# Performance work log

Measured on AMD Instinct MI355X. Metric: run time of the kernel, lower is better.

Reference implementation:

```python
import jax, jax.numpy as jnp
import numpy as np

D_MODEL = 1024
NUM_HEADS = 16
HEAD_DIM = D_MODEL // NUM_HEADS
D_FF = 4 * D_MODEL


def _linear_params(key, d_in, d_out):
    kw, kb = jax.random.split(key)
    bound = 1.0 / np.sqrt(d_in)
    W = jax.random.uniform(kw, (d_in, d_out), minval=-bound, maxval=bound, dtype=jnp.float32)
    b = jax.random.uniform(kb, (d_out,), minval=-bound, maxval=bound, dtype=jnp.float32)
    return W, b


def setup_inputs() -> dict:
    key = jax.random.key(0)
    ks = jax.random.split(key, 6)
    x = jax.random.normal(ks[0], (4, 2048, D_MODEL), dtype=jnp.float32)
    qkv_w, qkv_b = _linear_params(ks[1], D_MODEL, 3 * D_MODEL)
    out_w, out_b = _linear_params(ks[2], D_MODEL, D_MODEL)
    ffn1_w, ffn1_b = _linear_params(ks[3], D_MODEL, D_FF)
    ffn2_w, ffn2_b = _linear_params(ks[4], D_FF, D_MODEL)
    ln1_g = jnp.ones((D_MODEL,), jnp.float32); ln1_b = jnp.zeros((D_MODEL,), jnp.float32)
    ln2_g = jnp.ones((D_MODEL,), jnp.float32); ln2_b = jnp.zeros((D_MODEL,), jnp.float32)
    return {
        "x": x,
        "qkv_w": qkv_w, "qkv_b": qkv_b,
        "out_w": out_w, "out_b": out_b,
        "ffn1_w": ffn1_w, "ffn1_b": ffn1_b,
        "ffn2_w": ffn2_w, "ffn2_b": ffn2_b,
        "ln1_g": ln1_g, "ln1_b": ln1_b,
        "ln2_g": ln2_g, "ln2_b": ln2_b,
    }


def _layer_norm(x, g, b, eps=1e-5):
    mu = jnp.mean(x, axis=-1, keepdims=True)
    var = jnp.mean(jnp.square(x - mu), axis=-1, keepdims=True)
    return (x - mu) * jax.lax.rsqrt(var + eps) * g + b


def reference(x, qkv_w, qkv_b, out_w, out_b, ffn1_w, ffn1_b, ffn2_w, ffn2_b,
              ln1_g, ln1_b, ln2_g, ln2_b):
    B, S, D = x.shape
    H, Hd = NUM_HEADS, HEAD_DIM
    normed = _layer_norm(x, ln1_g, ln1_b)
    qkv = normed @ qkv_w + qkv_b                      # [B,S,3D]
    qkv = qkv.reshape(B, S, 3, H, Hd)
    q = jnp.transpose(qkv[:, :, 0], (0, 2, 1, 3))     # [B,H,S,Hd]
    k = jnp.transpose(qkv[:, :, 1], (0, 2, 1, 3))
    v = jnp.transpose(qkv[:, :, 2], (0, 2, 1, 3))
    scores = jnp.einsum('bhqd,bhkd->bhqk', q, k) / np.sqrt(Hd).astype(np.float32)
    causal = jnp.tril(jnp.ones((S, S), dtype=bool))
    scores = jnp.where(causal[None, None], scores, -jnp.inf)
    attn = jax.nn.softmax(scores, axis=-1)
    attn_out = jnp.einsum('bhqk,bhkd->bhqd', attn, v)  # [B,H,S,Hd]
    attn_out = jnp.transpose(attn_out, (0, 2, 1, 3)).reshape(B, S, D)
    attn_out = attn_out @ out_w + out_b
    x = x + attn_out
    h = _layer_norm(x, ln2_g, ln2_b)
    h = jax.nn.gelu(h @ ffn1_w + ffn1_b, approximate=False)
    h = h @ ffn2_w + ffn2_b
    return x + h
```

## Files before the change

### kernel.cpp

```cpp
#include <hip/hip_runtime.h>
#include <hip/hip_bf16.h>
#include <math.h>

typedef __attribute__((ext_vector_type(8))) short short8;
typedef __attribute__((ext_vector_type(4))) float f32x4;

__device__ __forceinline__ float bf2f(unsigned short u) {
    union { unsigned int i; float f; } c; c.i = ((unsigned int)u) << 16; return c.f;
}
__device__ __forceinline__ unsigned short f2bf(float f) {
    union { float f; unsigned int i; } c; c.f = f;
    unsigned int i = c.i;
    unsigned int r = (i + 0x7FFFu + ((i >> 16) & 1u)) >> 16;
    return (unsigned short)r;
}
__device__ __forceinline__ float fexp2(float x) { return __builtin_amdgcn_exp2f(x); }

__device__ __forceinline__ void gload16(const unsigned short* g, unsigned short* l) {
    __builtin_amdgcn_global_load_lds(
        (const __attribute__((address_space(1))) unsigned int*)g,
        (__attribute__((address_space(3))) unsigned int*)l, 16, 0, 0);
}

__device__ __forceinline__ void load8(const unsigned short* p, float* v) {
    short8 s = *(const short8*)p;
#pragma unroll
    for (int i = 0; i < 8; i++) v[i] = bf2f((unsigned short)s[i]);
}
__device__ __forceinline__ void load8(const float* p, float* v) {
    f32x4 a = ((const f32x4*)p)[0], b = ((const f32x4*)p)[1];
    v[0] = a[0]; v[1] = a[1]; v[2] = a[2]; v[3] = a[3];
    v[4] = b[0]; v[5] = b[1]; v[6] = b[2]; v[7] = b[3];
}
__device__ __forceinline__ void store8(unsigned short* p, const float* v) {
    short8 s;
#pragma unroll
    for (int i = 0; i < 8; i++) s[i] = (short)f2bf(v[i]);
    *(short8*)p = s;
}
__device__ __forceinline__ void store8(float* p, const float* v) {
    f32x4 a, b;
    a[0] = v[0]; a[1] = v[1]; a[2] = v[2]; a[3] = v[3];
    b[0] = v[4]; b[1] = v[5]; b[2] = v[6]; b[3] = v[7];
    ((f32x4*)p)[0] = a; ((f32x4*)p)[1] = b;
}

__global__ __launch_bounds__(256) void ln_f32_kernel(
    const float* __restrict__ x, const float* __restrict__ g,
    const float* __restrict__ b, unsigned short* __restrict__ out) {
    const int row = blockIdx.x;
    const int t = threadIdx.x;
    const float* xr = x + (size_t)row * 1024;
    float4 raw = ((const float4*)xr)[t];
    float v0 = raw.x, v1 = raw.y, v2 = raw.z, v3 = raw.w;
    float s = v0 + v1 + v2 + v3;
    float ss = v0 * v0 + v1 * v1 + v2 * v2 + v3 * v3;
    for (int off = 32; off > 0; off >>= 1) {
        s += __shfl_down(s, off);
        ss += __shfl_down(ss, off);
    }
    __shared__ float red[8];
    __shared__ float stat[2];
    const int wave = t >> 6, lane = t & 63;
    if (lane == 0) { red[wave] = s; red[4 + wave] = ss; }
    __syncthreads();
    if (t == 0) {
        float st = red[0] + red[1] + red[2] + red[3];
        float sst = red[4] + red[5] + red[6] + red[7];
        float mu = st * (1.0f / 1024.0f);
        float var = sst * (1.0f / 1024.0f) - mu * mu;
        stat[0] = mu; stat[1] = rsqrtf(var + 1e-5f);
    }
    __syncthreads();
    const float mu = stat[0], rstd = stat[1];
    float4 gr = ((const float4*)g)[t];
    float4 br = ((const float4*)b)[t];
    ushort4 o;
    o.x = f2bf((v0 - mu) * rstd * gr.x + br.x);
    o.y = f2bf((v1 - mu) * rstd * gr.y + br.y);
    o.z = f2bf((v2 - mu) * rstd * gr.z + br.z);
    o.w = f2bf((v3 - mu) * rstd * gr.w + br.w);
    ((ushort4*)(out + (size_t)row * 1024))[t] = o;
}

__global__ __launch_bounds__(256) void ln_bf16_kernel(
    const unsigned short* __restrict__ x, const float* __restrict__ g,
    const float* __restrict__ b, unsigned short* __restrict__ out) {
    const int row = blockIdx.x;
    const int t = threadIdx.x;
    const unsigned short* xr = x + (size_t)row * 1024;
    ushort4 raw = ((const ushort4*)xr)[t];
    float v0 = bf2f(raw.x), v1 = bf2f(raw.y), v2 = bf2f(raw.z), v3 = bf2f(raw.w);
    float s = v0 + v1 + v2 + v3;
    float ss = v0 * v0 + v1 * v1 + v2 * v2 + v3 * v3;
    for (int off = 32; off > 0; off >>= 1) {
        s += __shfl_down(s, off);
        ss += __shfl_down(ss, off);
    }
    __shared__ float red[8];
    __shared__ float stat[2];
    const int wave = t >> 6, lane = t & 63;
    if (lane == 0) { red[wave] = s; red[4 + wave] = ss; }
    __syncthreads();
    if (t == 0) {
        float st = red[0] + red[1] + red[2] + red[3];
        float sst = red[4] + red[5] + red[6] + red[7];
        float mu = st * (1.0f / 1024.0f);
        float var = sst * (1.0f / 1024.0f) - mu * mu;
        stat[0] = mu; stat[1] = rsqrtf(var + 1e-5f);
    }
    __syncthreads();
    const float mu = stat[0], rstd = stat[1];
    float4 gr = ((const float4*)g)[t];
    float4 br = ((const float4*)b)[t];
    ushort4 o;
    o.x = f2bf((v0 - mu) * rstd * gr.x + br.x);
    o.y = f2bf((v1 - mu) * rstd * gr.y + br.y);
    o.z = f2bf((v2 - mu) * rstd * gr.z + br.z);
    o.w = f2bf((v3 - mu) * rstd * gr.w + br.w);
    ((ushort4*)(out + (size_t)row * 1024))[t] = o;
}

__global__ __launch_bounds__(256) void transpose_cast_kernel(
    const float* __restrict__ in, unsigned short* __restrict__ out, int R, int C) {
    __shared__ unsigned short tile[32][33];
    const int bx = blockIdx.x * 32, by = blockIdx.y * 32;
    const int tx = threadIdx.x & 31, ty = threadIdx.x >> 5;
    for (int i = 0; i < 32; i += 8)
        tile[ty + i][tx] = f2bf(in[(size_t)(by + ty + i) * C + bx + tx]);
    __syncthreads();
    for (int i = 0; i < 32; i += 8)
        out[(size_t)(bx + ty + i) * R + by + tx] = tile[tx][ty + i];
}

enum { EPI_QKV = 0, EPI_RES = 1, EPI_GELU = 2 };

template <int EPI, typename RT, typename OT>
__global__ __launch_bounds__(256) void gemm_bt(
    const unsigned short* __restrict__ A, const unsigned short* __restrict__ Bt,
    const float* __restrict__ bias, const RT* __restrict__ res,
    OT* __restrict__ o0, unsigned short* __restrict__ o1,
    unsigned short* __restrict__ o2, int M, int N, int K) {
    constexpr int LE = 136;
    __shared__ __align__(16) unsigned short SMEM[17408];
    const int t = threadIdx.x;
    const int wave = t >> 6, lane = t & 63;
    const int lr = lane & 15, lq = lane >> 4;
    const int wm = (wave >> 1) * 64, wn = (wave & 1) * 64;
    const int m0 = blockIdx.y * 128, n0 = blockIdx.x * 128;
    f32x4 acc[4][4] = {};
    const int arow = t >> 2, acol = (t & 3) << 3;
    const unsigned short* ag = A + (size_t)(m0 + arow) * K + acol;
    const unsigned short* bg = Bt + (size_t)(n0 + arow) * K + acol;
    const size_t rstride = (size_t)64 * K;
    const int t8 = t * 8;
    {
        unsigned short* As = SMEM;
        unsigned short* Bs = SMEM + 4096;
        gload16(ag, As + t8);
        gload16(ag + rstride, As + 2048 + t8);
        gload16(bg, Bs + t8);
        gload16(bg + rstride, Bs + 2048 + t8);
    }
    const int nit = K >> 5;
    for (int it = 0; it < nit; ++it) {
        __syncthreads();
        if (it + 1 < nit) {
            const int nbuf = ((it + 1) & 1) * 8192;
            const int k0 = (it + 1) << 5;
            unsigned short* As = SMEM + nbuf;
            unsigned short* Bs = SMEM + nbuf + 4096;
            gload16(ag + k0, As + t8);
            gload16(ag + rstride + k0, As + 2048 + t8);
            gload16(bg + k0, Bs + t8);
            gload16(bg + rstride + k0, Bs + 2048 + t8);
        }
        const unsigned short* As = SMEM + (it & 1) * 8192;
        const unsigned short* Bs = As + 4096;
        short8 af[4], bfr[4];
#pragma unroll
        for (int i = 0; i < 4; i++) af[i] = *(const short8*)(As + (wm + i * 16 + lr) * 32 + lq * 8);
#pragma unroll
        for (int i = 0; i < 4; i++) bfr[i] = *(const short8*)(Bs + (wn + i * 16 + lr) * 32 + lq * 8);
#pragma unroll
        for (int mi = 0; mi < 4; mi++)
#pragma unroll
            for (int ni = 0; ni < 4; ni++)
                acc[mi][ni] = __builtin_amdgcn_mfma_f32_16x16x32_bf16(af[mi], bfr[ni], acc[mi][ni], 0, 0, 0);
    }
    __syncthreads();
    const bool vreg = (EPI == EPI_QKV) && (n0 >= 2048);
#pragma unroll
    for (int ni = 0; ni < 4; ni++) {
        const int col = wn + ni * 16 + lr;
        const float bv = bias[n0 + col];
#pragma unroll
        for (int mi = 0; mi < 4; mi++) {
#pragma unroll
            for (int r = 0; r < 4; r++) {
                const int row = wm + mi * 16 + lq * 4 + r;
                float val = acc[mi][ni][r] + bv;
                if (EPI == EPI_GELU)
                    val = 0.5f * val * (1.0f + erff(val * 0.70710678118654752f));
                if (vreg) SMEM[col * LE + row] = f2bf(val);
                else      SMEM[row * LE + col] = f2bf(val);
            }
        }
    }
    __syncthreads();
    const int rr = t >> 1, half = (t & 1) * 64;
    if (EPI == EPI_RES || EPI == EPI_GELU) {
        const size_t base = (size_t)(m0 + rr) * N + n0 + half;
        const unsigned short* src = SMEM + rr * LE + half;
#pragma unroll
        for (int j = 0; j < 8; j++) {
            float v[8];
            load8(src + j * 8, v);
            if (EPI == EPI_RES) {
                float rv[8];
                load8(res + base + j * 8, rv);
#pragma unroll
                for (int i = 0; i < 8; i++) v[i] += rv[i];
            }
            store8(o0 + base + j * 8, v);
        }
    } else if (!vreg) {
        const int gcol0 = n0 + half;
        const int which = gcol0 >> 10;
        const int hn = (gcol0 & 1023) >> 6;
        const int grow = m0 + rr;
        const size_t bh = (size_t)((grow >> 11) * 16 + hn);
        unsigned short* dst = (which == 0) ? (unsigned short*)o0 : o1;
        dst += (bh * 2048 + (grow & 2047)) * 64;
        const unsigned short* src = SMEM + rr * LE + half;
#pragma unroll
        for (int j = 0; j < 8; j++)
            *(short8*)(dst + j * 8) = *(const short8*)(src + j * 8);
    } else {
        const int c = rr;
        const int rem = (n0 + c) - 2048;
        const int hn = rem >> 6, d = rem & 63;
        const size_t bh = (size_t)((m0 >> 11) * 16 + hn);
        unsigned short* dst = o2 + (bh * 64 + d) * 2048 + (m0 & 2047) + half;
        const unsigned short* src = SMEM + c * LE + half;
#pragma unroll
        for (int j = 0; j < 8; j++)
            *(short8*)(dst + j * 8) = *(const short8*)(src + j * 8);
    }
}

__global__ __launch_bounds__(256) void attn_kernel(
    const unsigned short* __restrict__ qb, const unsigned short* __restrict__ kb,
    const unsigned short* __restrict__ vtb, unsigned short* __restrict__ aout) {
    const int bx = blockIdx.x;
    const int bh = blockIdx.y;
    const int bidx = bh >> 4, h = bh & 15;
    const int t = threadIdx.x, wave = t >> 6, lane = t & 63;
    const int lr = lane & 15, lq = lane >> 4;
    __shared__ __align__(16) unsigned short Ks[64 * 68];
    __shared__ __align__(16) unsigned short Vs[64 * 68];
    __shared__ __align__(16) unsigned short Ps[4][32 * 68];
    const unsigned short* kbase = kb + (size_t)bh * 2048 * 64;
    const unsigned short* vbase = vtb + (size_t)bh * 64 * 2048;
    const int srow = t >> 3, scol = (t & 7) * 8;
    const float kQScale = 0.125f * 1.44269504088896f;

    for (int phase = 0; phase < 2; phase++) {
        const int qblk = phase ? (15 - bx) : bx;
        const unsigned short* qbase = qb + ((size_t)bh * 2048 + qblk * 128 + wave * 32) * 64;
        short8 qf[2][2];
#pragma unroll
        for (int f = 0; f < 2; f++)
#pragma unroll
            for (int c = 0; c < 2; c++) {
                short8 raw = *(const short8*)(qbase + (f * 16 + lr) * 64 + c * 32 + lq * 8);
                short8 sc;
#pragma unroll
                for (int j = 0; j < 8; j++)
                    sc[j] = (short)f2bf(bf2f((unsigned short)raw[j]) * kQScale);
                qf[f][c] = sc;
            }
        f32x4 acc[2][4] = {};
        float m_i[2][4], l_i[2][4];
#pragma unroll
        for (int f = 0; f < 2; f++)
#pragma unroll
            for (int r = 0; r < 4; r++) { m_i[f][r] = -1e30f; l_i[f][r] = 0.0f; }
        const int wave_q0 = qblk * 128 + wave * 32;
        const int nkt = 2 * (qblk + 1);
        short8 kr0 = *(const short8*)(kbase + t * 8);
        short8 kr1 = *(const short8*)(kbase + 2048 + t * 8);
        short8 vr0 = *(const short8*)(vbase + (size_t)srow * 2048 + scol);
        short8 vr1 = *(const short8*)(vbase + (size_t)(32 + srow) * 2048 + scol);
        for (int kt = 0; kt < nkt; kt++) {
            __syncthreads();
            *(short8*)(Ks + srow * 68 + scol) = kr0;
            *(short8*)(Ks + (32 + srow) * 68 + scol) = kr1;
            *(short8*)(Vs + srow * 68 + scol) = vr0;
            *(short8*)(Vs + (32 + srow) * 68 + scol) = vr1;
            __syncthreads();
            if (kt + 1 < nkt) {
                const unsigned short* kg = kbase + (kt + 1) * 4096;
                kr0 = *(const short8*)(kg + t * 8);
                kr1 = *(const short8*)(kg + 2048 + t * 8);
                vr0 = *(const short8*)(vbase + (size_t)srow * 2048 + (kt + 1) * 64 + scol);
                vr1 = *(const short8*)(vbase + (size_t)(32 + srow) * 2048 + (kt + 1) * 64 + scol);
            }
            if (kt * 64 <= wave_q0 + 31) {
                f32x4 sa[2][4];
#pragma unroll
                for (int ni = 0; ni < 4; ni++) {
                    short8 kf0 = *(const short8*)(Ks + (ni * 16 + lr) * 68 + lq * 8);
                    short8 kf1 = *(const short8*)(Ks + (ni * 16 + lr) * 68 + 32 + lq * 8);
#pragma unroll
                    for (int f = 0; f < 2; f++) {
                        f32x4 z = {};
                        z = __builtin_amdgcn_mfma_f32_16x16x32_bf16(qf[f][0], kf0, z, 0, 0, 0);
                        sa[f][ni] = __builtin_amdgcn_mfma_f32_16x16x32_bf16(qf[f][1], kf1, z, 0, 0, 0);
                    }
                }
                const bool needmask = (kt * 64 + 63 > wave_q0);
                if (needmask) {
#pragma unroll
                    for (int f = 0; f < 2; f++) {
                        const int qrow0 = wave_q0 + f * 16 + lq * 4;
#pragma unroll
                        for (int ni = 0; ni < 4; ni++) {
                            const int kcol = kt * 64 + ni * 16 + lr;
#pragma unroll
                            for (int r = 0; r < 4; r++)
                                if (kcol > qrow0 + r) sa[f][ni][r] = -1e30f;
                        }
                    }
                }
#pragma unroll
                for (int f = 0; f < 2; f++) {
                    float mcur[4], alpha[4], rsum[4];
#pragma unroll
                    for (int r = 0; r < 4; r++)
                        mcur[r] = fmaxf(fmaxf(sa[f][0][r], sa[f][1][r]), fmaxf(sa[f][2][r], sa[f][3][r]));
#pragma unroll
                    for (int r = 0; r < 4; r++) {
#pragma unroll
                        for (int off = 1; off < 16; off <<= 1) mcur[r] = fmaxf(mcur[r], __shfl_xor(mcur[r], off));
                        const float mn = fmaxf(m_i[f][r], mcur[r]);
                        alpha[r] = fexp2(m_i[f][r] - mn);
                        m_i[f][r] = mn;
                        rsum[r] = 0.0f;
                    }
#pragma unroll
                    for (int ni = 0; ni < 4; ni++)
#pragma unroll
                        for (int r = 0; r < 4; r++) {
                            const float p = fexp2(sa[f][ni][r] - m_i[f][r]);
                            Ps[wave][(f * 16 + lq * 4 + r) * 68 + ni * 16 + lr] = f2bf(p);
                            rsum[r] += p;
                        }
#pragma unroll
                    for (int r = 0; r < 4; r++) {
#pragma unroll
                        for (int off = 1; off < 16; off <<= 1) rsum[r] += __shfl_xor(rsum[r], off);
                        l_i[f][r] = l_i[f][r] * alpha[r] + rsum[r];
#pragma unroll
                        for (int ni = 0; ni < 4; ni++) acc[f][ni][r] *= alpha[r];
                    }
                }
                short8 pf[2][2];
#pragma unroll
                for (int f = 0; f < 2; f++)
#pragma unroll
                    for (int c = 0; c < 2; c++)
                        pf[f][c] = *(const short8*)(&Ps[wave][(f * 16 + lr) * 68 + c * 32 + lq * 8]);
#pragma unroll
                for (int ni = 0; ni < 4; ni++) {
                    short8 vf0 = *(const short8*)(Vs + (ni * 16 + lr) * 68 + lq * 8);
                    short8 vf1 = *(const short8*)(Vs + (ni * 16 + lr) * 68 + 32 + lq * 8);
#pragma unroll
                    for (int f = 0; f < 2; f++) {
                        acc[f][ni] = __builtin_amdgcn_mfma_f32_16x16x32_bf16(pf[f][0], vf0, acc[f][ni], 0, 0, 0);
                        acc[f][ni] = __builtin_amdgcn_mfma_f32_16x16x32_bf16(pf[f][1], vf1, acc[f][ni], 0, 0, 0);
                    }
                }
            }
        }
#pragma unroll
        for (int f = 0; f < 2; f++)
#pragma unroll
            for (int r = 0; r < 4; r++) {
                const float rinv = 1.0f / l_i[f][r];
                const int q = qblk * 128 + wave * 32 + f * 16 + lq * 4 + r;
                const size_t token = (size_t)bidx * 2048 + q;
#pragma unroll
                for (int ni = 0; ni < 4; ni++)
                    aout[token * 1024 + h * 64 + ni * 16 + lr] = f2bf(acc[f][ni][r] * rinv);
            }
    }
}

extern "C" void kernel_launch(void* const* d_in, const int* in_sizes, int n_in,
                              void* d_out, int out_size, void* d_ws, size_t ws_size,
                              hipStream_t stream) {
    const float* x      = (const float*)d_in[0];
    const float* qkv_w  = (const float*)d_in[1];
    const float* qkv_b  = (const float*)d_in[2];
    const float* out_w  = (const float*)d_in[3];
    const float* out_b  = (const float*)d_in[4];
    const float* ffn1_w = (const float*)d_in[5];
    const float* ffn1_b = (const float*)d_in[6];
    const float* ffn2_w = (const float*)d_in[7];
    const float* ffn2_b = (const float*)d_in[8];
    const float* ln1_g  = (const float*)d_in[9];
    const float* ln1_b  = (const float*)d_in[10];
    const float* ln2_g  = (const float*)d_in[11];
    const float* ln2_b  = (const float*)d_in[12];
    float* out = (float*)d_out;
    char* W = (char*)d_ws;

    unsigned short* normed = (unsigned short*)(W);
    unsigned short* x1     = (unsigned short*)(W + 16777216);
    unsigned short* qbuf   = (unsigned short*)(W + 33554432);
    unsigned short* kbuf   = (unsigned short*)(W + 50331648);
    unsigned short* vbuf   = (unsigned short*)(W + 67108864);
    unsigned short* attnb  = (unsigned short*)(W + 83886080);
    unsigned short* hff    = (unsigned short*)(W + 33554432);
    unsigned short* qkv_wt = (unsigned short*)(W + 100663296);
    unsigned short* out_wt = (unsigned short*)(W + 106954752);
    unsigned short* f1_wt  = (unsigned short*)(W + 109051904);
    unsigned short* f2_wt  = (unsigned short*)(W + 117440512);

    transpose_cast_kernel<<<dim3(3072 / 32, 1024 / 32), 256, 0, stream>>>(qkv_w, qkv_wt, 1024, 3072);
    transpose_cast_kernel<<<dim3(1024 / 32, 1024 / 32), 256, 0, stream>>>(out_w, out_wt, 1024, 1024);
    transpose_cast_kernel<<<dim3(4096 / 32, 1024 / 32), 256, 0, stream>>>(ffn1_w, f1_wt, 1024, 4096);
    transpose_cast_kernel<<<dim3(1024 / 32, 4096 / 32), 256, 0, stream>>>(ffn2_w, f2_wt, 4096, 1024);

    ln_f32_kernel<<<dim3(8192), 256, 0, stream>>>(x, ln1_g, ln1_b, normed);
    gemm_bt<EPI_QKV, float, unsigned short><<<dim3(3072 / 128, 8192 / 128), 256, 0, stream>>>(
        normed, qkv_wt, qkv_b, nullptr, qbuf, kbuf, vbuf, 8192, 3072, 1024);
    attn_kernel<<<dim3(8, 64), 256, 0, stream>>>(qbuf, kbuf, vbuf, attnb);
    gemm_bt<EPI_RES, float, unsigned short><<<dim3(1024 / 128, 8192 / 128), 256, 0, stream>>>(
        attnb, out_wt, out_b, x, x1, nullptr, nullptr, 8192, 1024, 1024);
    ln_bf16_kernel<<<dim3(8192), 256, 0, stream>>>(x1, ln2_g, ln2_b, normed);
    gemm_bt<EPI_GELU, float, unsigned short><<<dim3(4096 / 128, 8192 / 128), 256, 0, stream>>>(
        normed, f1_wt, ffn1_b, nullptr, hff, nullptr, nullptr, 8192, 4096, 1024);
    gemm_bt<EPI_RES, unsigned short, float><<<dim3(1024 / 128, 8192 / 128), 256, 0, stream>>>(
        hff, f2_wt, ffn2_b, x1, out, nullptr, nullptr, 8192, 1024, 4096);
}
```

Measured before the change: 604.8 us.

## Replace GEMM with 256-row tiled, swizzled, ping-pong scheduled 512-thread kernel

Replaces the 128x128 GEMM with a 256xBN tile kernel using 8 waves, a K-step of 64, XOR-swizzled LDS layout and a barrier-interleaved schedule that alternates LDS reads with MFMA quadrants under raised wave priority. Larger tiles increase data reuse per global load, and the swizzle is meant to cut LDS bank conflicts. The epilogue is split into two halves so it fits in the reused shared memory. The cost is higher register and LDS pressure, more barriers, and fewer blocks for the N=1024 GEMMs.

```diff
diff --git a/kernel.cpp b/kernel.cpp
--- a/kernel.cpp
+++ b/kernel.cpp
@@ -135,117 +135,164 @@
 
 enum { EPI_QKV = 0, EPI_RES = 1, EPI_GELU = 2 };
 
-template <int EPI, typename RT, typename OT>
-__global__ __launch_bounds__(256) void gemm_bt(
+template <int BN, int EPI, typename RT, typename OT>
+__global__ __launch_bounds__(512, 2) void gemm256(
     const unsigned short* __restrict__ A, const unsigned short* __restrict__ Bt,
     const float* __restrict__ bias, const RT* __restrict__ res,
     OT* __restrict__ o0, unsigned short* __restrict__ o1,
     unsigned short* __restrict__ o2, int M, int N, int K) {
-    constexpr int LE = 136;
-    __shared__ __align__(16) unsigned short SMEM[17408];
+    constexpr int NFRAG = BN / 64;
+    constexpr int NF2 = NFRAG / 2;
+    constexpr int BQ = BN / 64;
+    constexpr int ASZ = 16384;
+    constexpr int BSZ = BN * 64;
+    constexpr int BUFSH = ASZ + BSZ;
+    constexpr int PE = BN + 8;
+    __shared__ __align__(16) unsigned short SMEM[2 * BUFSH];
     const int t = threadIdx.x;
     const int wave = t >> 6, lane = t & 63;
     const int lr = lane & 15, lq = lane >> 4;
-    const int wm = (wave >> 1) * 64, wn = (wave & 1) * 64;
-    const int m0 = blockIdx.y * 128, n0 = blockIdx.x * 128;
-    f32x4 acc[4][4] = {};
-    const int arow = t >> 2, acol = (t & 3) << 3;
-    const unsigned short* ag = A + (size_t)(m0 + arow) * K + acol;
-    const unsigned short* bg = Bt + (size_t)(n0 + arow) * K + acol;
-    const size_t rstride = (size_t)64 * K;
-    const int t8 = t * 8;
-    {
-        unsigned short* As = SMEM;
-        unsigned short* Bs = SMEM + 4096;
-        gload16(ag, As + t8);
-        gload16(ag + rstride, As + 2048 + t8);
-        gload16(bg, Bs + t8);
-        gload16(bg + rstride, Bs + 2048 + t8);
-    }
-    const int nit = K >> 5;
-    for (int it = 0; it < nit; ++it) {
+    const int wm = wave >> 2, wn = wave & 3;
+    const int m0 = blockIdx.y * 256, n0 = blockIdx.x * BN;
+    const int swz16 = (lr & 4) << 2;
+    f32x4 acc[8][NFRAG] = {};
+    short8 a[4][2], b[NF2][2];
+    const int tswz = (t * 16) ^ (((t >> 5) & 1) << 5);
+    const int srow = tswz >> 7;
+    const int scol = (tswz & 127) >> 1;
+    const unsigned short* agS = A + (size_t)(m0 + srow) * K + scol;
+    const unsigned short* bgS = Bt + (size_t)(n0 + srow) * K + scol;
+    const size_t q64K = (size_t)64 * K;
+
+#define STAGE(ktv, dv) do {                                                   \
+    unsigned short* dA_ = SMEM + (dv) * BUFSH;                                \
+    unsigned short* dB_ = dA_ + ASZ;                                          \
+    const int ko_ = (ktv) << 6;                                               \
+    _Pragma("unroll") for (int qi = 0; qi < 4; ++qi)                          \
+        gload16(agS + (size_t)qi * q64K + ko_, dA_ + qi * 4096 + t * 8);      \
+    _Pragma("unroll") for (int qi = 0; qi < BQ; ++qi)                         \
+        gload16(bgS + (size_t)qi * q64K + ko_, dB_ + qi * 4096 + t * 8);      \
+} while (0)
+
+#define READ_A(qm) do {                                                       \
+    _Pragma("unroll") for (int mi = 0; mi < 4; ++mi) {                        \
+        const int rA_ = wm * 128 + (qm) * 64 + mi * 16 + lr;                  \
+        _Pragma("unroll") for (int ks = 0; ks < 2; ++ks)                      \
+            a[mi][ks] = *(const short8*)(Ash + ((rA_ * 64 + ks * 32 + lq * 8) ^ swz16)); \
+    } } while (0)
+
+#define READ_B(qn) do {                                                       \
+    _Pragma("unroll") for (int ni = 0; ni < NF2; ++ni) {                      \
+        const int rB_ = wn * (BN / 4) + (qn) * (BN / 8) + ni * 16 + lr;       \
+        _Pragma("unroll") for (int ks = 0; ks < 2; ++ks)                      \
+            b[ni][ks] = *(const short8*)(Bsh + ((rB_ * 64 + ks * 32 + lq * 8) ^ swz16)); \
+    } } while (0)
+
+#define MFMAQ(qm, qn) do {                                                    \
+    _Pragma("unroll") for (int mi = 0; mi < 4; ++mi)                          \
+        _Pragma("unroll") for (int ni = 0; ni < NF2; ++ni) {                  \
+            f32x4 c_ = acc[(qm) * 4 + mi][(qn) * NF2 + ni];                   \
+            c_ = __builtin_amdgcn_mfma_f32_16x16x32_bf16(a[mi][0], b[ni][0], c_, 0, 0, 0); \
+            c_ = __builtin_amdgcn_mfma_f32_16x16x32_bf16(a[mi][1], b[ni][1], c_, 0, 0, 0); \
+            acc[(qm) * 4 + mi][(qn) * NF2 + ni] = c_;                         \
+        } } while (0)
+
+    STAGE(0, 0);
+    const int nkt = K >> 6;
+    for (int kt = 0; kt < nkt; ++kt) {
+        const unsigned short* Ash = SMEM + (kt & 1) * BUFSH;
+        const unsigned short* Bsh = Ash + ASZ;
+        asm volatile("s_waitcnt vmcnt(0)" ::: "memory");
+        __builtin_amdgcn_s_barrier();
+        __builtin_amdgcn_sched_barrier(0);
+        READ_A(0);
+        READ_B(0);
+        if (kt + 1 < nkt) { STAGE(kt + 1, (kt + 1) & 1); }
+        __builtin_amdgcn_s_barrier();
+        __builtin_amdgcn_s_setprio(1); MFMAQ(0, 0); __builtin_amdgcn_s_setprio(0);
+        __builtin_amdgcn_s_barrier();
+        READ_B(1);
+        __builtin_amdgcn_s_barrier();
+        __builtin_amdgcn_s_setprio(1); MFMAQ(0, 1); __builtin_amdgcn_s_setprio(0);
+        __builtin_amdgcn_s_barrier();
+        READ_A(1);
+        __builtin_amdgcn_s_barrier();
+        __builtin_amdgcn_s_setprio(1); MFMAQ(1, 1); __builtin_amdgcn_s_setprio(0);
+        __builtin_amdgcn_s_barrier();
+        READ_B(0);
+        __builtin_amdgcn_s_barrier();
+        __builtin_amdgcn_s_setprio(1); MFMAQ(1, 0); __builtin_amdgcn_s_setprio(0);
+    }
+#undef STAGE
+#undef READ_A
+#undef READ_B
+#undef MFMAQ
+
+    __syncthreads();
+    const bool vreg = (EPI == EPI_QKV) && (n0 >= 2048);
+    for (int h = 0; h < 2; ++h) {
+        if (h) __syncthreads();
+        if (wm == h) {
+#pragma unroll
+            for (int nj = 0; nj < NFRAG; ++nj) {
+                const int col = wn * (BN / 4) + nj * 16 + lr;
+                const float bv = bias[n0 + col];
+#pragma unroll
+                for (int mi = 0; mi < 8; ++mi) {
+#pragma unroll
+                    for (int r = 0; r < 4; ++r) {
+                        const int lrow = mi * 16 + lq * 4 + r;
+                        float val = acc[mi][nj][r] + bv;
+                        if (EPI == EPI_GELU)
+                            val = 0.5f * val * (1.0f + erff(val * 0.70710678118654752f));
+                        if (vreg) SMEM[col * 136 + lrow] = f2bf(val);
+                        else      SMEM[lrow * PE + col] = f2bf(val);
+                    }
+                }
+            }
+        }
         __syncthreads();
-        if (it + 1 < nit) {
-            const int nbuf = ((it + 1) & 1) * 8192;
-            const int k0 = (it + 1) << 5;
-            unsigned short* As = SMEM + nbuf;
-            unsigned short* Bs = SMEM + nbuf + 4096;
-            gload16(ag + k0, As + t8);
-            gload16(ag + rstride + k0, As + 2048 + t8);
-            gload16(bg + k0, Bs + t8);
-            gload16(bg + rstride + k0, Bs + 2048 + t8);
+        if (EPI == EPI_RES || EPI == EPI_GELU) {
+            const int rr = t >> 2, sg = (t & 3) * (BN / 4);
+            const size_t base = (size_t)(m0 + h * 128 + rr) * N + n0 + sg;
+            const unsigned short* src = SMEM + rr * PE + sg;
+#pragma unroll
+            for (int j = 0; j < BN / 32; ++j) {
+                float v[8];
+                load8(src + j * 8, v);
+                if (EPI == EPI_RES) {
+                    float rv[8];
+                    load8(res + base + j * 8, rv);
+#pragma unroll
+                    for (int i = 0; i < 8; i++) v[i] += rv[i];
+                }
+                store8(o0 + base + j * 8, v);
+            }
+        } else if (!vreg) {
+            const int rr = t >> 2, sg = (t & 3) * 64;
+            const int col0 = n0 + sg;
+            const int which = col0 >> 10;
+            const int hn = (col0 & 1023) >> 6;
+            const int grow = m0 + h * 128 + rr;
+            const size_t bh = (size_t)((grow >> 11) * 16 + hn);
+            unsigned short* dst = ((which == 0) ? (unsigned short*)o0 : o1) +
+                                  (bh * 2048 + (size_t)(grow & 2047)) * 64;
+            const unsigned short* src = SMEM + rr * PE + sg;
+#pragma unroll
+            for (int j = 0; j < 8; ++j)
+                *(short8*)(dst + j * 8) = *(const short8*)(src + j * 8);
+        } else {
+            const int c = t >> 1, rh = (t & 1) * 64;
+            const int rem = n0 + c - 2048;
+            const int hn = rem >> 6, dd = rem & 63;
+            const size_t bh = (size_t)((m0 >> 11) * 16 + hn);
+            unsigned short* dst = o2 + (bh * 64 + dd) * 2048 +
+                                  (size_t)((m0 + h * 128 + rh) & 2047);
+            const unsigned short* src = SMEM + c * 136 + rh;
+#pragma unroll
+            for (int j = 0; j < 8; ++j)
+                *(short8*)(dst + j * 8) = *(const short8*)(src + j * 8);
         }
-        const unsigned short* As = SMEM + (it & 1) * 8192;
-        const unsigned short* Bs = As + 4096;
-        short8 af[4], bfr[4];
-#pragma unroll
-        for (int i = 0; i < 4; i++) af[i] = *(const short8*)(As + (wm + i * 16 + lr) * 32 + lq * 8);
-#pragma unroll
-        for (int i = 0; i < 4; i++) bfr[i] = *(const short8*)(Bs + (wn + i * 16 + lr) * 32 + lq * 8);
-#pragma unroll
-        for (int mi = 0; mi < 4; mi++)
-#pragma unroll
-            for (int ni = 0; ni < 4; ni++)
-                acc[mi][ni] = __builtin_amdgcn_mfma_f32_16x16x32_bf16(af[mi], bfr[ni], acc[mi][ni], 0, 0, 0);
-    }
-    __syncthreads();
-    const bool vreg = (EPI == EPI_QKV) && (n0 >= 2048);
-#pragma unroll
-    for (int ni = 0; ni < 4; ni++) {
-        const int col = wn + ni * 16 + lr;
-        const float bv = bias[n0 + col];
-#pragma unroll
-        for (int mi = 0; mi < 4; mi++) {
-#pragma unroll
-            for (int r = 0; r < 4; r++) {
-                const int row = wm + mi * 16 + lq * 4 + r;
-                float val = acc[mi][ni][r] + bv;
-                if (EPI == EPI_GELU)
-                    val = 0.5f * val * (1.0f + erff(val * 0.70710678118654752f));
-                if (vreg) SMEM[col * LE + row] = f2bf(val);
-                else      SMEM[row * LE + col] = f2bf(val);
-            }
-        }
-    }
-    __syncthreads();
-    const int rr = t >> 1, half = (t & 1) * 64;
-    if (EPI == EPI_RES || EPI == EPI_GELU) {
-        const size_t base = (size_t)(m0 + rr) * N + n0 + half;
-        const unsigned short* src = SMEM + rr * LE + half;
-#pragma unroll
-        for (int j = 0; j < 8; j++) {
-            float v[8];
-            load8(src + j * 8, v);
-            if (EPI == EPI_RES) {
-                float rv[8];
-                load8(res + base + j * 8, rv);
-#pragma unroll
-                for (int i = 0; i < 8; i++) v[i] += rv[i];
-            }
-            store8(o0 + base + j * 8, v);
-        }
-    } else if (!vreg) {
-        const int gcol0 = n0 + half;
-        const int which = gcol0 >> 10;
-        const int hn = (gcol0 & 1023) >> 6;
-        const int grow = m0 + rr;
-        const size_t bh = (size_t)((grow >> 11) * 16 + hn);
-        unsigned short* dst = (which == 0) ? (unsigned short*)o0 : o1;
-        dst += (bh * 2048 + (grow & 2047)) * 64;
-        const unsigned short* src = SMEM + rr * LE + half;
-#pragma unroll
-        for (int j = 0; j < 8; j++)
-            *(short8*)(dst + j * 8) = *(const short8*)(src + j * 8);
-    } else {
-        const int c = rr;
-        const int rem = (n0 + c) - 2048;
-        const int hn = rem >> 6, d = rem & 63;
-        const size_t bh = (size_t)((m0 >> 11) * 16 + hn);
-        unsigned short* dst = o2 + (bh * 64 + d) * 2048 + (m0 & 2047) + half;
-        const unsigned short* src = SMEM + c * LE + half;
-#pragma unroll
-        for (int j = 0; j < 8; j++)
-            *(short8*)(dst + j * 8) = *(const short8*)(src + j * 8);
     }
 }
 
@@ -434,14 +481,14 @@
     transpose_cast_kernel<<<dim3(1024 / 32, 4096 / 32), 256, 0, stream>>>(ffn2_w, f2_wt, 4096, 1024);
 
     ln_f32_kernel<<<dim3(8192), 256, 0, stream>>>(x, ln1_g, ln1_b, normed);
-    gemm_bt<EPI_QKV, float, unsigned short><<<dim3(3072 / 128, 8192 / 128), 256, 0, stream>>>(
+    gemm256<256, EPI_QKV, float, unsigned short><<<dim3(3072 / 256, 8192 / 256), 512, 0, stream>>>(
         normed, qkv_wt, qkv_b, nullptr, qbuf, kbuf, vbuf, 8192, 3072, 1024);
     attn_kernel<<<dim3(8, 64), 256, 0, stream>>>(qbuf, kbuf, vbuf, attnb);
-    gemm_bt<EPI_RES, float, unsigned short><<<dim3(1024 / 128, 8192 / 128), 256, 0, stream>>>(
+    gemm256<128, EPI_RES, float, unsigned short><<<dim3(1024 / 128, 8192 / 256), 512, 0, stream>>>(
         attnb, out_wt, out_b, x, x1, nullptr, nullptr, 8192, 1024, 1024);
     ln_bf16_kernel<<<dim3(8192), 256, 0, stream>>>(x1, ln2_g, ln2_b, normed);
-    gemm_bt<EPI_GELU, float, unsigned short><<<dim3(4096 / 128, 8192 / 128), 256, 0, stream>>>(
+    gemm256<256, EPI_GELU, float, unsigned short><<<dim3(4096 / 256, 8192 / 256), 512, 0, stream>>>(
         normed, f1_wt, ffn1_b, nullptr, hff, nullptr, nullptr, 8192, 4096, 1024);
-    gemm_bt<EPI_RES, unsigned short, float><<<dim3(1024 / 128, 8192 / 128), 256, 0, stream>>>(
+    gemm256<128, EPI_RES, unsigned short, float><<<dim3(1024 / 128, 8192 / 256), 512, 0, stream>>>(
         hff, f2_wt, ffn2_b, x1, out, nullptr, nullptr, 8192, 1024, 4096);
 }
```

New measurement: 651.2 us. +7.7%, slower.
